# Performance work log

Hardware: AMD Instinct MI355X
Metric: run time of the kernel (lower is better)

The kernel has to match this reference:

```python
import jax, jax.numpy as jnp
import numpy as np

D_MODEL = 2048
D_STATE = 64
D_CONV = 4
EXPAND = 2
HEADDIM = 64
NGROUPS = 1
CHUNK = 64
D_INNER = D_MODEL * EXPAND          # 4096
NHEADS = D_INNER // HEADDIM         # 64
D_IN_PROJ = 2 * D_INNER + 2 * NGROUPS * D_STATE + NHEADS
BATCH, SEQLEN = 2, 4096
RMS_EPS = 1e-6


def elu_plus_one(x):
    return jax.nn.elu(x) + 1.0


def softplus(x):
    return jnp.where(x > 20, x, jnp.log1p(jnp.exp(x)))


def causal_conv1d(x, w, b):
    # x: (B, L, D), w: (K, D) depthwise kernel, b: (D,)
    Bsz, L, Dn = x.shape
    k = w.shape[0]
    xp = jnp.transpose(jnp.pad(x, ((0, 0), (k - 1, 0), (0, 0))), (0, 2, 1))  # (B, D, L+K-1)
    kern = jnp.transpose(w, (1, 0))[:, None, :]  # (D, 1, K)
    y = jax.lax.conv_general_dilated(xp, kern, (1,), 'VALID',
                                     feature_group_count=Dn,
                                     dimension_numbers=('NCH', 'OIH', 'NCH'))
    return jnp.transpose(y, (0, 2, 1)) + b


def ssd_chunked(q, k, v, a, chunk_size):
    # SSD / chunked linear attention with per-step scalar decay.
    # Recurrence: h_t = a_t * h_{t-1} + k_t v_t^T ; y_t = q_t @ h_t
    # q,k: (B,H,L,N); v: (B,H,L,P); a: (B,H,L) in (0,1)
    Bsz, H, L, N = q.shape
    S = chunk_size
    C = L // S
    qc = q.reshape(Bsz, H, C, S, N)
    kc = k.reshape(Bsz, H, C, S, N)
    vc = v.reshape(Bsz, H, C, S, -1)
    la = jnp.log(a).reshape(Bsz, H, C, S)
    cs = jnp.cumsum(la, axis=-1)                 # inclusive cumsum of log-decay within chunk
    causal = jnp.tril(jnp.ones((S, S), bool))
    # decay from position j to i (j<=i): exp(cs_i - cs_j)
    logdec = jnp.where(causal, cs[..., :, None] - cs[..., None, :], -jnp.inf)
    att = jnp.einsum('bhcsn,bhctn->bhcst', qc, kc) * jnp.exp(logdec)
    y_intra = jnp.einsum('bhcst,bhctp->bhcsp', att, vc)
    total = cs[..., -1]                           # (B,H,C) total log-decay per chunk
    k_scaled = kc * jnp.exp(total[..., None, None] - cs[..., None])
    states = jnp.einsum('bhcsn,bhcsp->bhcnp', k_scaled, vc)  # per-chunk state update
    d_t = jnp.moveaxis(jnp.exp(total), 2, 0)      # (C,B,H)
    s_t = jnp.moveaxis(states, 2, 0)              # (C,B,H,N,P)

    def step(h, inp):
        d, s = inp
        return d[..., None, None] * h + s, h      # emit state at chunk start

    _, h_prev = jax.lax.scan(step, jnp.zeros_like(s_t[0]), (d_t, s_t))
    h_prev = jnp.moveaxis(h_prev, 0, 2)           # (B,H,C,N,P)
    y_inter = jnp.einsum('bhcsn,bhcnp->bhcsp', qc * jnp.exp(cs)[..., None], h_prev)
    return (y_intra + y_inter).reshape(Bsz, H, L, -1)


def setup_inputs() -> dict:
    key = jax.random.key(0)
    k0, k1, k2, k3 = jax.random.split(key, 4)
    u = jax.random.normal(k0, (BATCH, SEQLEN, D_MODEL), jnp.float32)
    in_proj_w = jax.random.normal(k1, (D_MODEL, D_IN_PROJ), jnp.float32) / np.sqrt(D_MODEL)
    conv_weight = jax.random.normal(k2, (D_CONV, D_INNER), jnp.float32) / np.sqrt(D_CONV)
    conv_bias = jnp.zeros((D_INNER,), jnp.float32)
    A_log = jnp.log(jnp.linspace(1.0, 16.0, NHEADS)).astype(jnp.float32)
    dt_init = jnp.exp(jnp.linspace(np.log(0.001), np.log(0.1), NHEADS))
    dt_bias = (dt_init + jnp.log(-jnp.expm1(-dt_init))).astype(jnp.float32)
    D_param = jnp.ones((NHEADS,), jnp.float32)
    norm_scale = jnp.ones((D_INNER,), jnp.float32)
    out_proj_w = jax.random.normal(k3, (D_INNER, D_MODEL), jnp.float32) / np.sqrt(D_INNER)
    return dict(u=u, in_proj_w=in_proj_w, conv_weight=conv_weight, conv_bias=conv_bias,
                A_log=A_log, dt_bias=dt_bias, D_param=D_param, norm_scale=norm_scale,
                out_proj_w=out_proj_w)


def reference(u, in_proj_w, conv_weight, conv_bias, A_log, dt_bias, D_param, norm_scale, out_proj_w):
    Bsz, L, _ = u.shape
    zxBCdt = u @ in_proj_w
    splits = [D_INNER, 2 * D_INNER, 2 * D_INNER + NGROUPS * D_STATE, 2 * D_INNER + 2 * NGROUPS * D_STATE]
    z, x, B_proj, C_proj, dt_logits = jnp.split(zxBCdt, splits, axis=-1)
    x = jax.nn.silu(causal_conv1d(x, conv_weight, conv_bias))
    B_mat = elu_plus_one(B_proj.reshape(Bsz, L, NGROUPS, D_STATE))
    C_mat = elu_plus_one(C_proj.reshape(Bsz, L, NGROUPS, D_STATE))
    hpg = NHEADS // NGROUPS
    B_mat = jnp.repeat(B_mat, hpg, axis=2)   # (B,L,H,N)
    C_mat = jnp.repeat(C_mat, hpg, axis=2)
    dt = softplus(dt_logits + dt_bias)        # (B,L,H)
    a = jnp.exp(-dt * jnp.exp(A_log))         # (B,L,H), per-step decay
    x_heads = x.reshape(Bsz, L, NHEADS, HEADDIM)
    q = jnp.transpose(C_mat, (0, 2, 1, 3))
    k = jnp.transpose(B_mat, (0, 2, 1, 3))
    v = jnp.transpose(x_heads, (0, 2, 1, 3))
    a_t = jnp.transpose(a, (0, 2, 1))
    y = ssd_chunked(q, k, v, a_t, CHUNK)
    y = y + D_param[None, :, None, None] * v  # skip connection
    y = jnp.transpose(y, (0, 2, 1, 3)).reshape(Bsz, L, D_INNER)
    y = y * jax.lax.rsqrt(jnp.mean(y * y, axis=-1, keepdims=True) + RMS_EPS) * norm_scale
    y = y * jax.nn.silu(z)
    return y @ out_proj_w
```

## Files before the change

kernel.cpp:

```cpp
#include <hip/hip_runtime.h>
#include <hip/hip_bf16.h>
#include <cstdint>
#include <cstddef>

#define BATCH   2
#define SEQLEN  4096
#define DMODEL  2048
#define DINNER  4096
#define NHEADS  64
#define HEADDIM 64
#define DSTATE  64
#define CHUNK   64
#define NCHUNK  (SEQLEN/CHUNK)
#define DPROJ   8384
#define DPROJ_PAD 8448
#define MTOK    (BATCH*SEQLEN)
#define RMS_EPS 1e-6f

typedef __hip_bfloat16 bf16;
typedef __attribute__((ext_vector_type(8))) short bf16x8;
typedef __attribute__((ext_vector_type(4))) float f32x4;

__device__ __forceinline__ float siluf(float x) { return x / (1.f + expf(-x)); }
__device__ __forceinline__ float to_f(float x) { return x; }
__device__ __forceinline__ float to_f(bf16 x) { return __bfloat162float(x); }
__device__ __forceinline__ float bf2f(short s) { bf16 h; *(short*)&h = s; return __bfloat162float(h); }
__device__ __forceinline__ void from_f(float& d, float x) { d = x; }
__device__ __forceinline__ void from_f(bf16& d, float x) { d = __float2bfloat16(x); }

__device__ __forceinline__ void gload16(const void* g, void* l) {
  __builtin_amdgcn_global_load_lds(
      (const __attribute__((address_space(1))) void*)g,
      (__attribute__((address_space(3))) void*)l, 16, 0, 0);
}

template <int KT>
__global__ __launch_bounds__(1024, 4) void gemm_w16(
    const bf16* __restrict__ A, int lda,
    const bf16* __restrict__ BT, int ldb,
    bf16* __restrict__ C, int ldc, int gx) {
  __shared__ __align__(16) bf16 As[4 * 8192];
  __shared__ __align__(16) bf16 Bs[4 * 8192];
  const int tid  = threadIdx.x;
  const int lane = tid & 63;
  const int w    = tid >> 6;
  const int wm   = w >> 2;
  const int wn   = w & 3;
  const int lr   = lane & 15, lg = lane >> 4;
  const int fo   = 8 * (lg ^ ((lr >> 1) & 3));

  int nwg = gridDim.x;
  int bid = (int)blockIdx.x;
  int idx = (bid & 7) * (nwg >> 3) + (bid >> 3);
  int spos = idx % (8 * gx);
  const int m0 = ((idx / (8 * gx)) * 8 + (spos & 7)) * 256;
  const int n0 = (spos >> 3) * 256;

  const int srow = tid >> 2;
  const int ce   = 8 * ((tid & 3) ^ ((tid >> 3) & 3));
  const bf16* pA = A  + (size_t)(m0 + srow) * lda + ce;
  const bf16* pB = BT + (size_t)(n0 + srow) * ldb + ce;
  const int wofs = w * 512;
  const int aRd = (wm * 64 + lr) * 32 + fo;
  const int bRd = (wn * 64 + lr) * 32 + fo;

#define STAGE_A(kt) gload16(pA + ((kt) << 5), As + (((kt) & 3) << 13) + wofs)
#define STAGE_B(kt) gload16(pB + ((kt) << 5), Bs + (((kt) & 3) << 13) + wofs)

  f32x4 acc[4][4];
#pragma unroll
  for (int m = 0; m < 4; ++m)
#pragma unroll
    for (int n = 0; n < 4; ++n) acc[m][n] = (f32x4){0.f, 0.f, 0.f, 0.f};

#define KBODY(T, DOSTAGE, VMC) do {                                          \
    const bf16* Ab = As + (((T) & 3) << 13);                                 \
    const bf16* Bb = Bs + (((T) & 3) << 13);                                 \
    if (DOSTAGE) { STAGE_A((T) + 3); STAGE_B((T) + 3); }                     \
    bf16x8 bfv[4], af[4];                                                    \
    _Pragma("unroll")                                                        \
    for (int n = 0; n < 4; ++n) bfv[n] = *(const bf16x8*)&Bb[bRd + n * 512]; \
    _Pragma("unroll")                                                        \
    for (int m = 0; m < 4; ++m) af[m] = *(const bf16x8*)&Ab[aRd + m * 512];  \
    asm volatile("s_waitcnt lgkmcnt(0)" ::: "memory");                       \
    __builtin_amdgcn_sched_barrier(0);                                       \
    __builtin_amdgcn_s_setprio(1);                                           \
    _Pragma("unroll")                                                        \
    for (int m = 0; m < 4; ++m)                                              \
      _Pragma("unroll")                                                      \
      for (int n = 0; n < 4; ++n)                                            \
        acc[m][n] = __builtin_amdgcn_mfma_f32_16x16x32_bf16(af[m], bfv[n], acc[m][n], 0, 0, 0); \
    __builtin_amdgcn_s_setprio(0);                                           \
    asm volatile("s_waitcnt vmcnt(" #VMC ")" ::: "memory");                  \
    __builtin_amdgcn_s_barrier();                                            \
    __builtin_amdgcn_sched_barrier(0);                                       \
  } while (0)

  STAGE_A(0); STAGE_B(0); STAGE_A(1); STAGE_B(1); STAGE_A(2); STAGE_B(2);
  asm volatile("s_waitcnt vmcnt(4)" ::: "memory");
  __builtin_amdgcn_s_barrier();
  __builtin_amdgcn_sched_barrier(0);

#pragma unroll 4
  for (int t = 0; t < KT - 3; ++t) KBODY(t, true, 4);
  KBODY(KT - 3, false, 2);
  KBODY(KT - 2, false, 0);
  KBODY(KT - 1, false, 0);
#undef KBODY
#undef STAGE_A
#undef STAGE_B

  bf16* Ws = (w < 8 ? As : Bs) + (w & 7) * 4096;
#pragma unroll
  for (int m = 0; m < 4; ++m)
#pragma unroll
    for (int n = 0; n < 4; ++n)
#pragma unroll
      for (int reg = 0; reg < 4; ++reg) {
        int row = m * 16 + lg * 4 + reg;
        int slot = (n * 2 + (lr >> 3)) ^ (row & 7);
        Ws[row * 64 + slot * 8 + (lr & 7)] = __float2bfloat16(acc[m][n][reg]);
      }
  asm volatile("s_waitcnt lgkmcnt(0)" ::: "memory");
#pragma unroll
  for (int i = 0; i < 8; ++i) {
    int row = i * 8 + (lane >> 3);
    bf16x8 v = *(const bf16x8*)&Ws[row * 64 + ((lane & 7) ^ (lane >> 3)) * 8];
    int gcol = n0 + wn * 64 + (lane & 7) * 8;
    *(bf16x8*)&C[(size_t)(m0 + wm * 64 + row) * ldc + gcol] = v;
  }
}

template <typename TC, bool MASK, int KT>
__global__ __launch_bounds__(512, 2) void gemm_u(
    const bf16* __restrict__ A, int lda,
    const bf16* __restrict__ BT, int ldb,
    TC* __restrict__ C, int ldc, int Nvalid, int gx) {
  __shared__ __align__(16) bf16 As[4 * 8192];
  __shared__ __align__(16) bf16 Bs[4 * 8192];
  const int tid  = threadIdx.x;
  const int lane = tid & 63;
  const int w    = tid >> 6;
  const int wm   = w >> 2;
  const int wn   = w & 3;
  const int lr   = lane & 15, lg = lane >> 4;
  const int fo   = 8 * (lg ^ ((lr >> 1) & 3));

  int nwg = gridDim.x;
  int bid = (int)blockIdx.x;
  int idx = (bid & 7) * (nwg >> 3) + (bid >> 3);
  int spos = idx % (8 * gx);
  const int m0 = ((idx / (8 * gx)) * 8 + (spos & 7)) * 256;
  const int n0 = (spos >> 3) * 256;

  const int srow = tid >> 2;
  const int ce   = 8 * ((tid & 3) ^ ((tid >> 3) & 3));
  const bf16* pA0 = A  + (size_t)(m0 + srow)       * lda + ce;
  const bf16* pA1 = A  + (size_t)(m0 + 128 + srow) * lda + ce;
  const bf16* pB0 = BT + (size_t)(n0 + srow)       * ldb + ce;
  const bf16* pB1 = BT + (size_t)(n0 + 128 + srow) * ldb + ce;
  const int wofs = w * 512;
  const int aRd = (wm * 128 + lr) * 32 + fo;
  const int bRd = (wn * 64 + lr) * 32 + fo;

#define STAGE_A(kt) do {                                       \
    bf16* d_ = As + (((kt) & 3) << 13);  int kk_ = (kt) << 5;  \
    gload16(pA0 + kk_, d_ + wofs);                             \
    gload16(pA1 + kk_, d_ + 4096 + wofs);                      \
  } while (0)
#define STAGE_B(kt) do {                                       \
    bf16* d_ = Bs + (((kt) & 3) << 13);  int kk_ = (kt) << 5;  \
    gload16(pB0 + kk_, d_ + wofs);                             \
    gload16(pB1 + kk_, d_ + 4096 + wofs);                      \
  } while (0)

  f32x4 acc[8][4];
#pragma unroll
  for (int m = 0; m < 8; ++m)
#pragma unroll
    for (int n = 0; n < 4; ++n) acc[m][n] = (f32x4){0.f, 0.f, 0.f, 0.f};

#define KBODY(T, DOSTAGE, VMC) do {                                          \
    const bf16* Ab = As + (((T) & 3) << 13);                                 \
    const bf16* Bb = Bs + (((T) & 3) << 13);                                 \
    if (DOSTAGE) { STAGE_A((T) + 3); STAGE_B((T) + 3); }                     \
    bf16x8 bfv[4], af[4], ag[4];                                             \
    _Pragma("unroll")                                                        \
    for (int n = 0; n < 4; ++n) bfv[n] = *(const bf16x8*)&Bb[bRd + n * 512]; \
    _Pragma("unroll")                                                        \
    for (int m = 0; m < 4; ++m) af[m] = *(const bf16x8*)&Ab[aRd + m * 512];  \
    __builtin_amdgcn_sched_barrier(0);                                       \
    _Pragma("unroll")                                                        \
    for (int m = 0; m < 4; ++m) ag[m] = *(const bf16x8*)&Ab[aRd + (m + 4) * 512]; \
    asm volatile("s_waitcnt lgkmcnt(4)" ::: "memory");                       \
    __builtin_amdgcn_sched_barrier(0);                                       \
    __builtin_amdgcn_s_setprio(1);                                           \
    _Pragma("unroll")                                                        \
    for (int m = 0; m < 4; ++m)                                              \
      _Pragma("unroll")                                                      \
      for (int n = 0; n < 4; ++n)                                            \
        acc[m][n] = __builtin_amdgcn_mfma_f32_16x16x32_bf16(af[m], bfv[n], acc[m][n], 0, 0, 0); \
    asm volatile("s_waitcnt lgkmcnt(0)" ::: "memory");                       \
    __builtin_amdgcn_sched_barrier(0);                                       \
    _Pragma("unroll")                                                        \
    for (int m = 0; m < 4; ++m)                                              \
      _Pragma("unroll")                                                      \
      for (int n = 0; n < 4; ++n)                                            \
        acc[m + 4][n] = __builtin_amdgcn_mfma_f32_16x16x32_bf16(ag[m], bfv[n], acc[m + 4][n], 0, 0, 0); \
    __builtin_amdgcn_s_setprio(0);                                           \
    asm volatile("s_waitcnt vmcnt(" #VMC ")" ::: "memory");                  \
    __builtin_amdgcn_s_barrier();                                            \
    __builtin_amdgcn_sched_barrier(0);                                       \
  } while (0)

  STAGE_A(0); STAGE_B(0); STAGE_A(1); STAGE_B(1); STAGE_A(2); STAGE_B(2);
  asm volatile("s_waitcnt vmcnt(8)" ::: "memory");
  __builtin_amdgcn_s_barrier();
  __builtin_amdgcn_sched_barrier(0);

#pragma unroll 4
  for (int t = 0; t < KT - 3; ++t) KBODY(t, true, 8);
  KBODY(KT - 3, false, 4);
  KBODY(KT - 2, false, 0);
  KBODY(KT - 1, false, 0);
#undef KBODY
#undef STAGE_A
#undef STAGE_B

  if constexpr (__is_same(TC, bf16)) {
    bf16* Ws = (w < 4 ? As : Bs) + (w & 3) * 8192;
#pragma unroll
    for (int m = 0; m < 8; ++m)
#pragma unroll
      for (int n = 0; n < 4; ++n)
#pragma unroll
        for (int reg = 0; reg < 4; ++reg) {
          int row = m * 16 + lg * 4 + reg;
          int slot = (n * 2 + (lr >> 3)) ^ (row & 7);
          Ws[row * 64 + slot * 8 + (lr & 7)] = __float2bfloat16(acc[m][n][reg]);
        }
    asm volatile("s_waitcnt lgkmcnt(0)" ::: "memory");
#pragma unroll
    for (int i = 0; i < 16; ++i) {
      int row = i * 8 + (lane >> 3);
      bf16x8 v = *(const bf16x8*)&Ws[row * 64 + ((lane & 7) ^ (lane >> 3)) * 8];
      int gcol = n0 + wn * 64 + (lane & 7) * 8;
      if (!MASK || gcol < Nvalid)
        *(bf16x8*)&((bf16*)C)[(size_t)(m0 + wm * 128 + row) * ldc + gcol] = v;
    }
  } else {
#pragma unroll
    for (int m = 0; m < 8; ++m)
#pragma unroll
      for (int n = 0; n < 4; ++n) {
        int col = n0 + wn * 64 + n * 16 + lr;
        if (MASK && col >= Nvalid) continue;
        size_t rbase = (size_t)(m0 + wm * 128 + m * 16 + lg * 4);
#pragma unroll
        for (int reg = 0; reg < 4; ++reg)
          from_f(C[(rbase + reg) * ldc + col], acc[m][n][reg]);
      }
  }
}

template <typename TC, bool MASK>
__global__ __launch_bounds__(256) void gemm_mfma(
    const bf16* __restrict__ A, int lda,
    const bf16* __restrict__ BT, int ldb,
    TC* __restrict__ C, int ldc, int Kdim, int Nvalid) {
  __shared__ __align__(16) bf16 As[128 * 32];
  __shared__ __align__(16) bf16 Bs[128 * 32];
  const int tid  = threadIdx.x;
  const int lane = tid & 63;
  const int w    = tid >> 6;
  const int m0 = blockIdx.y * 128;
  const int n0 = blockIdx.x * 128;

  const int rs0 = w * 32 + (lane >> 2);
  const int ce  = 8 * ((lane & 3) ^ ((lane >> 2) & 3));
  const int fo  = 8 * ((lane >> 4) ^ (lane & 3));
  const int lr  = lane & 15, lg = lane >> 4;
  const int wr = w >> 1, wc = w & 1;

  f32x4 acc[4][4];
#pragma unroll
  for (int m = 0; m < 4; ++m)
#pragma unroll
    for (int n = 0; n < 4; ++n) acc[m][n] = (f32x4){0.f, 0.f, 0.f, 0.f};

  const size_t arow0 = (size_t)(m0 + rs0) * lda;
  const size_t arow1 = (size_t)(m0 + rs0 + 16) * lda;
  const size_t brow0 = (size_t)(n0 + rs0) * ldb;
  const size_t brow1 = (size_t)(n0 + rs0 + 16) * ldb;
  bf16* lA0 = &As[(w * 2 + 0) * 512];
  bf16* lA1 = &As[(w * 2 + 1) * 512];
  bf16* lB0 = &Bs[(w * 2 + 0) * 512];
  bf16* lB1 = &Bs[(w * 2 + 1) * 512];

  for (int k0 = 0; k0 < Kdim; k0 += 32) {
    __syncthreads();
    gload16(A + arow0 + k0 + ce, lA0);
    gload16(A + arow1 + k0 + ce, lA1);
    gload16(BT + brow0 + k0 + ce, lB0);
    gload16(BT + brow1 + k0 + ce, lB1);
    __syncthreads();
    bf16x8 af[4], bfr[4];
#pragma unroll
    for (int m = 0; m < 4; ++m)
      af[m] = *(const bf16x8*)&As[(wr * 64 + m * 16 + lr) * 32 + fo];
#pragma unroll
    for (int n = 0; n < 4; ++n)
      bfr[n] = *(const bf16x8*)&Bs[(wc * 64 + n * 16 + lr) * 32 + fo];
#pragma unroll
    for (int m = 0; m < 4; ++m)
#pragma unroll
      for (int n = 0; n < 4; ++n)
        acc[m][n] = __builtin_amdgcn_mfma_f32_16x16x32_bf16(af[m], bfr[n], acc[m][n], 0, 0, 0);
  }

#pragma unroll
  for (int m = 0; m < 4; ++m)
#pragma unroll
    for (int n = 0; n < 4; ++n) {
      int col = n0 + wc * 64 + n * 16 + lr;
      if (MASK && col >= Nvalid) continue;
      size_t rbase = (size_t)(m0 + wr * 64 + m * 16 + lg * 4);
#pragma unroll
      for (int reg = 0; reg < 4; ++reg)
        from_f(C[(rbase + reg) * ldc + col], acc[m][n][reg]);
    }
}

__global__ __launch_bounds__(256) void cast_bf16_kernel(
    const float* __restrict__ x, bf16* __restrict__ y) {
  size_t i = ((size_t)blockIdx.x * 256 + threadIdx.x) * 4;
  float4 v = *(const float4*)(x + i);
  y[i + 0] = __float2bfloat16(v.x);
  y[i + 1] = __float2bfloat16(v.y);
  y[i + 2] = __float2bfloat16(v.z);
  y[i + 3] = __float2bfloat16(v.w);
}

__global__ __launch_bounds__(256) void transpose_cast_kernel(
    const float* __restrict__ W, bf16* __restrict__ WT, int N, int K) {
  __shared__ float t[32][33];
  int n0 = blockIdx.x * 32, k0 = blockIdx.y * 32;
  int tx = threadIdx.x & 31, ty = threadIdx.x >> 5;
#pragma unroll
  for (int i = 0; i < 4; ++i) {
    int n = n0 + tx;
    t[ty + i * 8][tx] = (n < N) ? W[(size_t)(k0 + ty + i * 8) * N + n] : 0.f;
  }
  __syncthreads();
#pragma unroll
  for (int i = 0; i < 4; ++i) {
    int nn = ty + i * 8;
    WT[(size_t)(n0 + nn) * K + k0 + tx] = __float2bfloat16(t[tx][nn]);
  }
}

__global__ __launch_bounds__(256) void conv_silu_kernel(
    const bf16* __restrict__ zx, const float* __restrict__ cw,
    const float* __restrict__ cb, bf16* __restrict__ xc) {
  int idx = blockIdx.x * 256 + threadIdx.x;
  int d8 = (idx & 511) * 8;
  int m = idx >> 9;
  int l = m & (SEQLEN - 1);
  int b = m >> 12;
  float acc[8];
#pragma unroll
  for (int j = 0; j < 8; ++j) acc[j] = cb[d8 + j];
#pragma unroll
  for (int k = 0; k < 4; ++k) {
    int li = l - 3 + k;
    if (li >= 0) {
      bf16x8 xv = *(const bf16x8*)&zx[(size_t)(b * SEQLEN + li) * DPROJ + DINNER + d8];
      const float* cwp = cw + k * DINNER + d8;
#pragma unroll
      for (int j = 0; j < 8; ++j) acc[j] += bf2f(xv[j]) * cwp[j];
    }
  }
  bf16x8 o;
#pragma unroll
  for (int j = 0; j < 8; ++j) { bf16 h = __float2bfloat16(siluf(acc[j])); o[j] = *(short*)&h; }
  *(bf16x8*)&xc[(size_t)m * DINNER + d8] = o;
}

__global__ __launch_bounds__(256) void prep_cumsum_kernel(
    const bf16* __restrict__ zx, const float* __restrict__ A_log,
    const float* __restrict__ dt_bias, bf16* __restrict__ Bmb,
    bf16* __restrict__ Cmb, float* __restrict__ cs) {
  int bid = blockIdx.x;
  int c = bid & 63, b = bid >> 6;
  int m0 = b * SEQLEN + c * CHUNK;
  int tid = threadIdx.x;
  int s = tid >> 2, grp = (tid & 3) * 16;
  __shared__ float laT[64 * 65];
  __shared__ float segs[4][64];
  const bf16* row = zx + (size_t)(m0 + s) * DPROJ + 2 * DINNER;
  {
    union { bf16x8 v[2]; bf16 hh[16]; } u, o;
    u.v[0] = *(const bf16x8*)&row[grp];
    u.v[1] = *(const bf16x8*)&row[grp + 8];
#pragma unroll
    for (int i = 0; i < 16; ++i) {
      float bv = to_f(u.hh[i]);
      from_f(o.hh[i], bv > 0.f ? bv + 1.f : expf(bv));
    }
    *(bf16x8*)&Bmb[(size_t)(m0 + s) * 64 + grp] = o.v[0];
    *(bf16x8*)&Bmb[(size_t)(m0 + s) * 64 + grp + 8] = o.v[1];
    u.v[0] = *(const bf16x8*)&row[64 + grp];
    u.v[1] = *(const bf16x8*)&row[64 + grp + 8];
#pragma unroll
    for (int i = 0; i < 16; ++i) {
      float cv = to_f(u.hh[i]);
      from_f(o.hh[i], cv > 0.f ? cv + 1.f : expf(cv));
    }
    *(bf16x8*)&Cmb[(size_t)(m0 + s) * 64 + grp] = o.v[0];
    *(bf16x8*)&Cmb[(size_t)(m0 + s) * 64 + grp + 8] = o.v[1];
    u.v[0] = *(const bf16x8*)&row[128 + grp];
    u.v[1] = *(const bf16x8*)&row[128 + grp + 8];
#pragma unroll
    for (int i = 0; i < 16; ++i) {
      int j = grp + i;
      float dtl = to_f(u.hh[i]) + dt_bias[j];
      float dt = dtl > 20.f ? dtl : log1pf(expf(dtl));
      laT[j * 65 + s] = -dt * expf(A_log[j]);
    }
  }
  __syncthreads();
  int j = tid & 63, sg = tid >> 6;
  float p = 0.f;
#pragma unroll
  for (int i = 0; i < 16; ++i) p += laT[j * 65 + sg * 16 + i];
  segs[sg][j] = p;
  __syncthreads();
  float off = (sg > 0 ? segs[0][j] : 0.f) + (sg > 1 ? segs[1][j] : 0.f) +
              (sg > 2 ? segs[2][j] : 0.f);
  float acc = off;
#pragma unroll
  for (int i = 0; i < 16; ++i) {
    acc += laT[j * 65 + sg * 16 + i];
    cs[(size_t)(m0 + sg * 16 + i) * 64 + j] = acc;
  }
}

__global__ __launch_bounds__(256) void states_mfma(
    const bf16* __restrict__ Bmb, const bf16* __restrict__ xc,
    const float* __restrict__ cs, bf16* __restrict__ st) {
  int bid = blockIdx.x;
  int c = bid & 63, h = (bid >> 6) & 63, b = bid >> 12;
  int m0 = b * SEQLEN + c * CHUNK;
  int tid = threadIdx.x, lane = tid & 63, w = tid >> 6;
  int lr = lane & 15, lg = lane >> 4;
  __shared__ bf16 vT[64 * 72];
  __shared__ bf16 kT[64 * 72];
  int s4 = tid >> 2, c16 = (tid & 3) * 16;
  float cstot = cs[(size_t)(m0 + 63) * 64 + h];
  float ws = expf(cstot - cs[(size_t)(m0 + s4) * 64 + h]);
  {
    union { bf16x8 v[2]; bf16 hh[16]; } u;
    const bf16x8* pv = (const bf16x8*)&xc[(size_t)(m0 + s4) * DINNER + h * 64 + c16];
    u.v[0] = pv[0]; u.v[1] = pv[1];
#pragma unroll
    for (int i = 0; i < 16; ++i) vT[(c16 + i) * 72 + s4] = u.hh[i];
    const bf16x8* pk = (const bf16x8*)&Bmb[(size_t)(m0 + s4) * 64 + c16];
    u.v[0] = pk[0]; u.v[1] = pk[1];
#pragma unroll
    for (int i = 0; i < 16; ++i) kT[(c16 + i) * 72 + s4] = __float2bfloat16(to_f(u.hh[i]) * ws);
  }
  __syncthreads();
  f32x4 acc[4];
#pragma unroll
  for (int ct = 0; ct < 4; ++ct) acc[ct] = (f32x4){0.f, 0.f, 0.f, 0.f};
#pragma unroll
  for (int ks = 0; ks < 2; ++ks) {
    bf16x8 af = *(const bf16x8*)&vT[(w * 16 + lr) * 72 + ks * 32 + lg * 8];
#pragma unroll
    for (int ct = 0; ct < 4; ++ct) {
      bf16x8 bf_ = *(const bf16x8*)&kT[(ct * 16 + lr) * 72 + ks * 32 + lg * 8];
      acc[ct] = __builtin_amdgcn_mfma_f32_16x16x32_bf16(af, bf_, acc[ct], 0, 0, 0);
    }
  }
  size_t ob = (((size_t)(b * NHEADS + h)) * NCHUNK + c) * 4096;
#pragma unroll
  for (int ct = 0; ct < 4; ++ct) {
    int n = ct * 16 + lr;
#pragma unroll
    for (int r = 0; r < 4; ++r) {
      int p = w * 16 + lg * 4 + r;
      from_f(st[ob + (size_t)p * 64 + n], acc[ct][r]);
    }
  }
}

__global__ __launch_bounds__(256) void scan_kernel(
    const float* __restrict__ cs, bf16* __restrict__ st) {
  int bid = blockIdx.x;
  int bh = bid >> 2, qq = bid & 3;
  int b = bh >> 6, h = bh & 63;
  int tid = threadIdx.x;
  __shared__ float dec[64];
  if (tid < 64)
    dec[tid] = expf(cs[(size_t)(b * SEQLEN + tid * CHUNK + 63) * 64 + h]);
  int e0 = qq * 1024 + tid * 4;
  float hr[4] = {0.f, 0.f, 0.f, 0.f};
  size_t base = (size_t)bh * NCHUNK * 4096;
  typedef __attribute__((ext_vector_type(4))) short bf16x4;
  union U { bf16x4 v; bf16 hh[4]; };
  U buf[4];
  buf[0].v = *(bf16x4*)(st + base + 0 * 4096 + e0);
  buf[1].v = *(bf16x4*)(st + base + 1 * 4096 + e0);
  buf[2].v = *(bf16x4*)(st + base + 2 * 4096 + e0);
  __syncthreads();
#pragma unroll 4
  for (int c = 0; c < NCHUNK; ++c) {
    if (c + 3 < NCHUNK)
      buf[(c + 3) & 3].v = *(bf16x4*)(st + base + (size_t)(c + 3) * 4096 + e0);
    float d = dec[c];
    U out;
#pragma unroll
    for (int i = 0; i < 4; ++i) {
      float sv = to_f(buf[c & 3].hh[i]);
      from_f(out.hh[i], hr[i]);
      hr[i] = d * hr[i] + sv;
    }
    *(bf16x4*)(st + base + (size_t)c * 4096 + e0) = out.v;
  }
}

__global__ __launch_bounds__(256) void chunk_out_mfma(
    const bf16* __restrict__ Bmb, const bf16* __restrict__ Cmb,
    const bf16* __restrict__ xc, const float* __restrict__ cs,
    const bf16* __restrict__ st, const float* __restrict__ Dp,
    bf16* __restrict__ zx) {
  int bid = blockIdx.x;
  int c = bid & 63, h = (bid >> 6) & 63, b = bid >> 12;
  int m0 = b * SEQLEN + c * CHUNK;
  int tid = threadIdx.x, lane = tid & 63, w = tid >> 6;
  int lr = lane & 15, lg = lane >> 4;
  __shared__ bf16 qL[64 * 72];
  __shared__ bf16 kL[64 * 72];
  __shared__ bf16 A2[64 * 136];
  __shared__ bf16 B2[64 * 136];
  __shared__ float csl[64];
  int s4 = tid >> 2, c16 = (tid & 3) * 16;

  if (tid < 64) csl[tid] = cs[(size_t)(m0 + tid) * 64 + h];
  {
    const bf16x8* pq = (const bf16x8*)&Cmb[(size_t)(m0 + s4) * 64 + c16];
    *(bf16x8*)&qL[s4 * 72 + c16] = pq[0];
    *(bf16x8*)&qL[s4 * 72 + c16 + 8] = pq[1];
    const bf16x8* pk = (const bf16x8*)&Bmb[(size_t)(m0 + s4) * 64 + c16];
    *(bf16x8*)&kL[s4 * 72 + c16] = pk[0];
    *(bf16x8*)&kL[s4 * 72 + c16 + 8] = pk[1];
  }
  {
    union { bf16x8 v[2]; bf16 hh[16]; } u;
    const bf16x8* pv = (const bf16x8*)&xc[(size_t)(m0 + s4) * DINNER + h * 64 + c16];
    u.v[0] = pv[0]; u.v[1] = pv[1];
#pragma unroll
    for (int i = 0; i < 16; ++i) B2[(c16 + i) * 136 + s4] = u.hh[i];
  }
  {
    size_t hb = (((size_t)(b * NHEADS + h)) * NCHUNK + c) * 4096;
    const bf16x8* ph = (const bf16x8*)&st[hb + (size_t)s4 * 64 + c16];
    *(bf16x8*)&B2[s4 * 136 + 64 + c16] = ph[0];
    *(bf16x8*)&B2[s4 * 136 + 64 + c16 + 8] = ph[1];
  }
  __syncthreads();

  f32x4 acc1[4];
#pragma unroll
  for (int ct = 0; ct < 4; ++ct) acc1[ct] = (f32x4){0.f, 0.f, 0.f, 0.f};
#pragma unroll
  for (int ks = 0; ks < 2; ++ks) {
    bf16x8 af = *(const bf16x8*)&qL[(w * 16 + lr) * 72 + ks * 32 + lg * 8];
#pragma unroll
    for (int ct = 0; ct < 4; ++ct) {
      bf16x8 bf_ = *(const bf16x8*)&kL[(ct * 16 + lr) * 72 + ks * 32 + lg * 8];
      acc1[ct] = __builtin_amdgcn_mfma_f32_16x16x32_bf16(af, bf_, acc1[ct], 0, 0, 0);
    }
  }
  {
    float es = expf(csl[s4]);
    union { bf16x8 v[2]; bf16 hh[16]; } u;
    const bf16x8* pq = (const bf16x8*)&qL[s4 * 72 + c16];
    u.v[0] = pq[0]; u.v[1] = pq[1];
#pragma unroll
    for (int i = 0; i < 16; ++i) u.hh[i] = __float2bfloat16(to_f(u.hh[i]) * es);
    *(bf16x8*)&A2[s4 * 136 + 64 + c16] = u.v[0];
    *(bf16x8*)&A2[s4 * 136 + 64 + c16 + 8] = u.v[1];
  }
#pragma unroll
  for (int ct = 0; ct < 4; ++ct) {
    int t = ct * 16 + lr;
#pragma unroll
    for (int r = 0; r < 4; ++r) {
      int s = w * 16 + lg * 4 + r;
      float val = (t <= s) ? acc1[ct][r] * expf(csl[s] - csl[t]) : 0.f;
      A2[s * 136 + t] = __float2bfloat16(val);
    }
  }
  __syncthreads();

  float Dh = Dp[h];
  f32x4 acc2[4];
#pragma unroll
  for (int ct = 0; ct < 4; ++ct) {
    int p = ct * 16 + lr;
#pragma unroll
    for (int r = 0; r < 4; ++r)
      acc2[ct][r] = Dh * to_f(B2[p * 136 + (w * 16 + lg * 4 + r)]);
  }
#pragma unroll
  for (int ks = 0; ks < 4; ++ks) {
    bf16x8 af = *(const bf16x8*)&A2[(w * 16 + lr) * 136 + ks * 32 + lg * 8];
#pragma unroll
    for (int ct = 0; ct < 4; ++ct) {
      bf16x8 bf_ = *(const bf16x8*)&B2[(ct * 16 + lr) * 136 + ks * 32 + lg * 8];
      acc2[ct] = __builtin_amdgcn_mfma_f32_16x16x32_bf16(af, bf_, acc2[ct], 0, 0, 0);
    }
  }
  __syncthreads();
#pragma unroll
  for (int ct = 0; ct < 4; ++ct) {
    int p = ct * 16 + lr;
#pragma unroll
    for (int r = 0; r < 4; ++r)
      qL[(w * 16 + lg * 4 + r) * 72 + p] = __float2bfloat16(acc2[ct][r]);
  }
  __syncthreads();
  {
    const bf16x8* py = (const bf16x8*)&qL[s4 * 72 + c16];
    bf16x8* pg = (bf16x8*)&zx[(size_t)(m0 + s4) * DPROJ + DINNER + h * 64 + c16];
    pg[0] = py[0]; pg[1] = py[1];
  }
}

__global__ __launch_bounds__(256) void rmsnorm_gate_kernel(
    bf16* __restrict__ zx, const float* __restrict__ scale) {
  int m = blockIdx.x;
  int tid = threadIdx.x;
  bf16* row = zx + (size_t)m * DPROJ;
  float vals[16];
  float ss = 0.f;
#pragma unroll
  for (int g = 0; g < 2; ++g) {
    int d8 = (tid + g * 256) * 8;
    bf16x8 yv = *(const bf16x8*)&row[DINNER + d8];
#pragma unroll
    for (int j = 0; j < 8; ++j) {
      float y = bf2f(yv[j]);
      vals[g * 8 + j] = y;
      ss += y * y;
    }
  }
#pragma unroll
  for (int off = 32; off > 0; off >>= 1) ss += __shfl_down(ss, off, 64);
  __shared__ float red[4];
  if ((tid & 63) == 0) red[tid >> 6] = ss;
  __syncthreads();
  float tot = red[0] + red[1] + red[2] + red[3];
  float inv = rsqrtf(tot / (float)DINNER + RMS_EPS);
#pragma unroll
  for (int g = 0; g < 2; ++g) {
    int d8 = (tid + g * 256) * 8;
    bf16x8 zv = *(const bf16x8*)&row[d8];
    const float* sc = scale + d8;
    bf16x8 o;
#pragma unroll
    for (int j = 0; j < 8; ++j) {
      bf16 hh = __float2bfloat16(vals[g * 8 + j] * inv * sc[j] * siluf(bf2f(zv[j])));
      o[j] = *(short*)&hh;
    }
    *(bf16x8*)&row[DINNER + d8] = o;
  }
}

extern "C" void kernel_launch(void* const* d_in, const int* in_sizes, int n_in,
                              void* d_out, int out_size, void* d_ws, size_t ws_size,
                              hipStream_t stream) {
  const float* u       = (const float*)d_in[0];
  const float* Win     = (const float*)d_in[1];
  const float* cw      = (const float*)d_in[2];
  const float* cb      = (const float*)d_in[3];
  const float* A_log   = (const float*)d_in[4];
  const float* dt_bias = (const float*)d_in[5];
  const float* Dp      = (const float*)d_in[6];
  const float* nscale  = (const float*)d_in[7];
  const float* Wout    = (const float*)d_in[8];
  float* out = (float*)d_out;

  bf16* zx = (bf16*)d_ws;
  bf16* xc = zx + (size_t)MTOK * DPROJ;
  bf16* ub = xc;
  bf16* wT = xc + (size_t)MTOK * DINNER;
  bf16* Bmb = wT + (size_t)DPROJ_PAD * DMODEL;
  bf16* Cmb = Bmb + (size_t)MTOK * 64;
  float* cs = (float*)(Cmb + (size_t)MTOK * 64);
  bf16* st = (bf16*)d_out;

  cast_bf16_kernel<<<(MTOK * DMODEL) / (256 * 4), 256, 0, stream>>>(u, ub);
  transpose_cast_kernel<<<dim3(DPROJ_PAD / 32, DMODEL / 32), 256, 0, stream>>>(Win, wT, DPROJ, DMODEL);
  gemm_w16<DMODEL / 32><<<(2 * DINNER / 256) * (MTOK / 256), 1024, 0, stream>>>(
      ub, DMODEL, wT, DMODEL, zx, DPROJ, 2 * DINNER / 256);
  gemm_mfma<bf16, true><<<dim3(2, MTOK / 128), 256, 0, stream>>>(
      ub, DMODEL, wT + (size_t)(2 * DINNER) * DMODEL, DMODEL,
      zx + 2 * DINNER, DPROJ, DMODEL, 192);
  transpose_cast_kernel<<<dim3(DMODEL / 32, DINNER / 32), 256, 0, stream>>>(Wout, wT, DMODEL, DINNER);
  conv_silu_kernel<<<(MTOK * 512) / 256, 256, 0, stream>>>(zx, cw, cb, xc);
  prep_cumsum_kernel<<<BATCH * NCHUNK, 256, 0, stream>>>(zx, A_log, dt_bias, Bmb, Cmb, cs);
  states_mfma<<<BATCH * NHEADS * NCHUNK, 256, 0, stream>>>(Bmb, xc, cs, st);
  scan_kernel<<<BATCH * NHEADS * 4, 256, 0, stream>>>(cs, st);
  chunk_out_mfma<<<BATCH * NHEADS * NCHUNK, 256, 0, stream>>>(Bmb, Cmb, xc, cs, st, Dp, zx);
  rmsnorm_gate_kernel<<<MTOK, 256, 0, stream>>>(zx, nscale);
  gemm_u<float, false, DINNER / 32><<<(DMODEL / 256) * (MTOK / 256), 512, 0, stream>>>(
      zx + DINNER, DPROJ, wT, DINNER, out, DMODEL, DMODEL, DMODEL / 256);
}
```

Baseline: 663.9 us.

## Double-buffer GEMM fragments, reuse 1024-thread GEMM for out-proj, tile conv rows

```diff
diff --git a/kernel.cpp b/kernel.cpp
--- a/kernel.cpp
+++ b/kernel.cpp
@@ -34,11 +34,11 @@
       (__attribute__((address_space(3))) void*)l, 16, 0, 0);
 }
 
-template <int KT>
+template <typename TC, int KT>
 __global__ __launch_bounds__(1024, 4) void gemm_w16(
     const bf16* __restrict__ A, int lda,
     const bf16* __restrict__ BT, int ldb,
-    bf16* __restrict__ C, int ldc, int gx) {
+    TC* __restrict__ C, int ldc, int gx) {
   __shared__ __align__(16) bf16 As[4 * 8192];
   __shared__ __align__(16) bf16 Bs[4 * 8192];
   const int tid  = threadIdx.x;
@@ -73,164 +73,62 @@
 #pragma unroll
     for (int n = 0; n < 4; ++n) acc[m][n] = (f32x4){0.f, 0.f, 0.f, 0.f};
 
-#define KBODY(T, DOSTAGE, VMC) do {                                          \
-    const bf16* Ab = As + (((T) & 3) << 13);                                 \
-    const bf16* Bb = Bs + (((T) & 3) << 13);                                 \
-    if (DOSTAGE) { STAGE_A((T) + 3); STAGE_B((T) + 3); }                     \
-    bf16x8 bfv[4], af[4];                                                    \
-    _Pragma("unroll")                                                        \
-    for (int n = 0; n < 4; ++n) bfv[n] = *(const bf16x8*)&Bb[bRd + n * 512]; \
-    _Pragma("unroll")                                                        \
-    for (int m = 0; m < 4; ++m) af[m] = *(const bf16x8*)&Ab[aRd + m * 512];  \
-    asm volatile("s_waitcnt lgkmcnt(0)" ::: "memory");                       \
-    __builtin_amdgcn_sched_barrier(0);                                       \
-    __builtin_amdgcn_s_setprio(1);                                           \
-    _Pragma("unroll")                                                        \
-    for (int m = 0; m < 4; ++m)                                              \
-      _Pragma("unroll")                                                      \
-      for (int n = 0; n < 4; ++n)                                            \
-        acc[m][n] = __builtin_amdgcn_mfma_f32_16x16x32_bf16(af[m], bfv[n], acc[m][n], 0, 0, 0); \
-    __builtin_amdgcn_s_setprio(0);                                           \
-    asm volatile("s_waitcnt vmcnt(" #VMC ")" ::: "memory");                  \
-    __builtin_amdgcn_s_barrier();                                            \
-    __builtin_amdgcn_sched_barrier(0);                                       \
+  bf16x8 fr[2][8];
+
+#define RDFRAG(P, SL) do {                                                    \
+    const bf16* Ab_ = As + ((SL) << 13);                                      \
+    const bf16* Bb_ = Bs + ((SL) << 13);                                      \
+    _Pragma("unroll")                                                         \
+    for (int n = 0; n < 4; ++n) fr[P][4 + n] = *(const bf16x8*)&Bb_[bRd + n * 512]; \
+    _Pragma("unroll")                                                         \
+    for (int m = 0; m < 4; ++m) fr[P][m] = *(const bf16x8*)&Ab_[aRd + m * 512]; \
+  } while (0)
+
+#define KB(T, P, DOSTAGE, DOPF, VMC) do {                                     \
+    if (DOSTAGE) { STAGE_A((T) + 3); STAGE_B((T) + 3); }                      \
+    asm volatile("s_waitcnt lgkmcnt(0)" ::: "memory");                        \
+    __builtin_amdgcn_sched_barrier(0);                                        \
+    __builtin_amdgcn_s_setprio(1);                                            \
+    _Pragma("unroll")                                                         \
+    for (int m = 0; m < 4; ++m)                                               \
+      _Pragma("unroll")                                                       \
+      for (int n = 0; n < 4; ++n)                                             \
+        acc[m][n] = __builtin_amdgcn_mfma_f32_16x16x32_bf16(fr[P][m], fr[P][4 + n], acc[m][n], 0, 0, 0); \
+    __builtin_amdgcn_s_setprio(0);                                            \
+    if (DOPF) {                                                               \
+      asm volatile("s_waitcnt vmcnt(" #VMC ")" ::: "memory");                 \
+      __builtin_amdgcn_sched_barrier(0);                                      \
+      RDFRAG(1 - (P), ((T) + 1) & 3);                                         \
+    }                                                                         \
+    __builtin_amdgcn_s_barrier();                                             \
+    __builtin_amdgcn_sched_barrier(0);                                        \
   } while (0)
 
   STAGE_A(0); STAGE_B(0); STAGE_A(1); STAGE_B(1); STAGE_A(2); STAGE_B(2);
   asm volatile("s_waitcnt vmcnt(4)" ::: "memory");
   __builtin_amdgcn_s_barrier();
   __builtin_amdgcn_sched_barrier(0);
-
-#pragma unroll 4
-  for (int t = 0; t < KT - 3; ++t) KBODY(t, true, 4);
-  KBODY(KT - 3, false, 2);
-  KBODY(KT - 2, false, 0);
-  KBODY(KT - 1, false, 0);
-#undef KBODY
+  RDFRAG(0, 0);
+
+  for (int t4 = 0; t4 < KT - 4; t4 += 4) {
+    KB(t4 + 0, 0, true, true, 4);
+    KB(t4 + 1, 1, true, true, 4);
+    KB(t4 + 2, 0, true, true, 4);
+    KB(t4 + 3, 1, true, true, 4);
+  }
+  KB(KT - 4, 0, true,  true,  4);
+  KB(KT - 3, 1, false, true,  2);
+  KB(KT - 2, 0, false, true,  0);
+  KB(KT - 1, 1, false, false, 0);
+#undef KB
+#undef RDFRAG
 #undef STAGE_A
 #undef STAGE_B
 
-  bf16* Ws = (w < 8 ? As : Bs) + (w & 7) * 4096;
-#pragma unroll
-  for (int m = 0; m < 4; ++m)
-#pragma unroll
-    for (int n = 0; n < 4; ++n)
-#pragma unroll
-      for (int reg = 0; reg < 4; ++reg) {
-        int row = m * 16 + lg * 4 + reg;
-        int slot = (n * 2 + (lr >> 3)) ^ (row & 7);
-        Ws[row * 64 + slot * 8 + (lr & 7)] = __float2bfloat16(acc[m][n][reg]);
-      }
-  asm volatile("s_waitcnt lgkmcnt(0)" ::: "memory");
-#pragma unroll
-  for (int i = 0; i < 8; ++i) {
-    int row = i * 8 + (lane >> 3);
-    bf16x8 v = *(const bf16x8*)&Ws[row * 64 + ((lane & 7) ^ (lane >> 3)) * 8];
-    int gcol = n0 + wn * 64 + (lane & 7) * 8;
-    *(bf16x8*)&C[(size_t)(m0 + wm * 64 + row) * ldc + gcol] = v;
-  }
-}
-
-template <typename TC, bool MASK, int KT>
-__global__ __launch_bounds__(512, 2) void gemm_u(
-    const bf16* __restrict__ A, int lda,
-    const bf16* __restrict__ BT, int ldb,
-    TC* __restrict__ C, int ldc, int Nvalid, int gx) {
-  __shared__ __align__(16) bf16 As[4 * 8192];
-  __shared__ __align__(16) bf16 Bs[4 * 8192];
-  const int tid  = threadIdx.x;
-  const int lane = tid & 63;
-  const int w    = tid >> 6;
-  const int wm   = w >> 2;
-  const int wn   = w & 3;
-  const int lr   = lane & 15, lg = lane >> 4;
-  const int fo   = 8 * (lg ^ ((lr >> 1) & 3));
-
-  int nwg = gridDim.x;
-  int bid = (int)blockIdx.x;
-  int idx = (bid & 7) * (nwg >> 3) + (bid >> 3);
-  int spos = idx % (8 * gx);
-  const int m0 = ((idx / (8 * gx)) * 8 + (spos & 7)) * 256;
-  const int n0 = (spos >> 3) * 256;
-
-  const int srow = tid >> 2;
-  const int ce   = 8 * ((tid & 3) ^ ((tid >> 3) & 3));
-  const bf16* pA0 = A  + (size_t)(m0 + srow)       * lda + ce;
-  const bf16* pA1 = A  + (size_t)(m0 + 128 + srow) * lda + ce;
-  const bf16* pB0 = BT + (size_t)(n0 + srow)       * ldb + ce;
-  const bf16* pB1 = BT + (size_t)(n0 + 128 + srow) * ldb + ce;
-  const int wofs = w * 512;
-  const int aRd = (wm * 128 + lr) * 32 + fo;
-  const int bRd = (wn * 64 + lr) * 32 + fo;
-
-#define STAGE_A(kt) do {                                       \
-    bf16* d_ = As + (((kt) & 3) << 13);  int kk_ = (kt) << 5;  \
-    gload16(pA0 + kk_, d_ + wofs);                             \
-    gload16(pA1 + kk_, d_ + 4096 + wofs);                      \
-  } while (0)
-#define STAGE_B(kt) do {                                       \
-    bf16* d_ = Bs + (((kt) & 3) << 13);  int kk_ = (kt) << 5;  \
-    gload16(pB0 + kk_, d_ + wofs);                             \
-    gload16(pB1 + kk_, d_ + 4096 + wofs);                      \
-  } while (0)
-
-  f32x4 acc[8][4];
-#pragma unroll
-  for (int m = 0; m < 8; ++m)
-#pragma unroll
-    for (int n = 0; n < 4; ++n) acc[m][n] = (f32x4){0.f, 0.f, 0.f, 0.f};
-
-#define KBODY(T, DOSTAGE, VMC) do {                                          \
-    const bf16* Ab = As + (((T) & 3) << 13);                                 \
-    const bf16* Bb = Bs + (((T) & 3) << 13);                                 \
-    if (DOSTAGE) { STAGE_A((T) + 3); STAGE_B((T) + 3); }                     \
-    bf16x8 bfv[4], af[4], ag[4];                                             \
-    _Pragma("unroll")                                                        \
-    for (int n = 0; n < 4; ++n) bfv[n] = *(const bf16x8*)&Bb[bRd + n * 512]; \
-    _Pragma("unroll")                                                        \
-    for (int m = 0; m < 4; ++m) af[m] = *(const bf16x8*)&Ab[aRd + m * 512];  \
-    __builtin_amdgcn_sched_barrier(0);                                       \
-    _Pragma("unroll")                                                        \
-    for (int m = 0; m < 4; ++m) ag[m] = *(const bf16x8*)&Ab[aRd + (m + 4) * 512]; \
-    asm volatile("s_waitcnt lgkmcnt(4)" ::: "memory");                       \
-    __builtin_amdgcn_sched_barrier(0);                                       \
-    __builtin_amdgcn_s_setprio(1);                                           \
-    _Pragma("unroll")                                                        \
-    for (int m = 0; m < 4; ++m)                                              \
-      _Pragma("unroll")                                                      \
-      for (int n = 0; n < 4; ++n)                                            \
-        acc[m][n] = __builtin_amdgcn_mfma_f32_16x16x32_bf16(af[m], bfv[n], acc[m][n], 0, 0, 0); \
-    asm volatile("s_waitcnt lgkmcnt(0)" ::: "memory");                       \
-    __builtin_amdgcn_sched_barrier(0);                                       \
-    _Pragma("unroll")                                                        \
-    for (int m = 0; m < 4; ++m)                                              \
-      _Pragma("unroll")                                                      \
-      for (int n = 0; n < 4; ++n)                                            \
-        acc[m + 4][n] = __builtin_amdgcn_mfma_f32_16x16x32_bf16(ag[m], bfv[n], acc[m + 4][n], 0, 0, 0); \
-    __builtin_amdgcn_s_setprio(0);                                           \
-    asm volatile("s_waitcnt vmcnt(" #VMC ")" ::: "memory");                  \
-    __builtin_amdgcn_s_barrier();                                            \
-    __builtin_amdgcn_sched_barrier(0);                                       \
-  } while (0)
-
-  STAGE_A(0); STAGE_B(0); STAGE_A(1); STAGE_B(1); STAGE_A(2); STAGE_B(2);
-  asm volatile("s_waitcnt vmcnt(8)" ::: "memory");
-  __builtin_amdgcn_s_barrier();
-  __builtin_amdgcn_sched_barrier(0);
-
-#pragma unroll 4
-  for (int t = 0; t < KT - 3; ++t) KBODY(t, true, 8);
-  KBODY(KT - 3, false, 4);
-  KBODY(KT - 2, false, 0);
-  KBODY(KT - 1, false, 0);
-#undef KBODY
-#undef STAGE_A
-#undef STAGE_B
-
   if constexpr (__is_same(TC, bf16)) {
-    bf16* Ws = (w < 4 ? As : Bs) + (w & 3) * 8192;
-#pragma unroll
-    for (int m = 0; m < 8; ++m)
+    bf16* Ws = (w < 8 ? As : Bs) + (w & 7) * 4096;
+#pragma unroll
+    for (int m = 0; m < 4; ++m)
 #pragma unroll
       for (int n = 0; n < 4; ++n)
 #pragma unroll
@@ -241,21 +139,19 @@
         }
     asm volatile("s_waitcnt lgkmcnt(0)" ::: "memory");
 #pragma unroll
-    for (int i = 0; i < 16; ++i) {
+    for (int i = 0; i < 8; ++i) {
       int row = i * 8 + (lane >> 3);
       bf16x8 v = *(const bf16x8*)&Ws[row * 64 + ((lane & 7) ^ (lane >> 3)) * 8];
       int gcol = n0 + wn * 64 + (lane & 7) * 8;
-      if (!MASK || gcol < Nvalid)
-        *(bf16x8*)&((bf16*)C)[(size_t)(m0 + wm * 128 + row) * ldc + gcol] = v;
+      *(bf16x8*)&((bf16*)C)[(size_t)(m0 + wm * 64 + row) * ldc + gcol] = v;
     }
   } else {
 #pragma unroll
-    for (int m = 0; m < 8; ++m)
+    for (int m = 0; m < 4; ++m)
 #pragma unroll
       for (int n = 0; n < 4; ++n) {
         int col = n0 + wn * 64 + n * 16 + lr;
-        if (MASK && col >= Nvalid) continue;
-        size_t rbase = (size_t)(m0 + wm * 128 + m * 16 + lg * 4);
+        size_t rbase = (size_t)(m0 + wm * 64 + m * 16 + lg * 4);
 #pragma unroll
         for (int reg = 0; reg < 4; ++reg)
           from_f(C[(rbase + reg) * ldc + col], acc[m][n][reg]);
@@ -364,26 +260,49 @@
     const float* __restrict__ cb, bf16* __restrict__ xc) {
   int idx = blockIdx.x * 256 + threadIdx.x;
   int d8 = (idx & 511) * 8;
-  int m = idx >> 9;
-  int l = m & (SEQLEN - 1);
-  int b = m >> 12;
-  float acc[8];
-#pragma unroll
-  for (int j = 0; j < 8; ++j) acc[j] = cb[d8 + j];
+  int g = idx >> 9;
+  int m0 = g * 4;
+  int l0 = m0 & (SEQLEN - 1);
+  int b = m0 >> 12;
+  bf16x8 rows[7];
+  bf16x8 zvec;
+#pragma unroll
+  for (int j = 0; j < 8; ++j) zvec[j] = 0;
+#pragma unroll
+  for (int r = 0; r < 7; ++r) {
+    int li = l0 - 3 + r;
+    rows[r] = (li >= 0)
+        ? *(const bf16x8*)&zx[(size_t)(b * SEQLEN + li) * DPROJ + DINNER + d8]
+        : zvec;
+  }
+  float cwv[4][8], cbv[8];
 #pragma unroll
   for (int k = 0; k < 4; ++k) {
-    int li = l - 3 + k;
-    if (li >= 0) {
-      bf16x8 xv = *(const bf16x8*)&zx[(size_t)(b * SEQLEN + li) * DPROJ + DINNER + d8];
-      const float* cwp = cw + k * DINNER + d8;
-#pragma unroll
-      for (int j = 0; j < 8; ++j) acc[j] += bf2f(xv[j]) * cwp[j];
-    }
-  }
-  bf16x8 o;
-#pragma unroll
-  for (int j = 0; j < 8; ++j) { bf16 h = __float2bfloat16(siluf(acc[j])); o[j] = *(short*)&h; }
-  *(bf16x8*)&xc[(size_t)m * DINNER + d8] = o;
+    float4 a = *(const float4*)(cw + k * DINNER + d8);
+    float4 bb = *(const float4*)(cw + k * DINNER + d8 + 4);
+    cwv[k][0] = a.x; cwv[k][1] = a.y; cwv[k][2] = a.z; cwv[k][3] = a.w;
+    cwv[k][4] = bb.x; cwv[k][5] = bb.y; cwv[k][6] = bb.z; cwv[k][7] = bb.w;
+  }
+  {
+    float4 a = *(const float4*)(cb + d8);
+    float4 bb = *(const float4*)(cb + d8 + 4);
+    cbv[0] = a.x; cbv[1] = a.y; cbv[2] = a.z; cbv[3] = a.w;
+    cbv[4] = bb.x; cbv[5] = bb.y; cbv[6] = bb.z; cbv[7] = bb.w;
+  }
+#pragma unroll
+  for (int j = 0; j < 4; ++j) {
+    float acc[8];
+#pragma unroll
+    for (int e = 0; e < 8; ++e) acc[e] = cbv[e];
+#pragma unroll
+    for (int k = 0; k < 4; ++k)
+#pragma unroll
+      for (int e = 0; e < 8; ++e) acc[e] += bf2f(rows[j + k][e]) * cwv[k][e];
+    bf16x8 o;
+#pragma unroll
+    for (int e = 0; e < 8; ++e) { bf16 h = __float2bfloat16(siluf(acc[e])); o[e] = *(short*)&h; }
+    *(bf16x8*)&xc[(size_t)(m0 + j) * DINNER + d8] = o;
+  }
 }
 
 __global__ __launch_bounds__(256) void prep_cumsum_kernel(
@@ -703,18 +622,18 @@
 
   cast_bf16_kernel<<<(MTOK * DMODEL) / (256 * 4), 256, 0, stream>>>(u, ub);
   transpose_cast_kernel<<<dim3(DPROJ_PAD / 32, DMODEL / 32), 256, 0, stream>>>(Win, wT, DPROJ, DMODEL);
-  gemm_w16<DMODEL / 32><<<(2 * DINNER / 256) * (MTOK / 256), 1024, 0, stream>>>(
+  gemm_w16<bf16, DMODEL / 32><<<(2 * DINNER / 256) * (MTOK / 256), 1024, 0, stream>>>(
       ub, DMODEL, wT, DMODEL, zx, DPROJ, 2 * DINNER / 256);
   gemm_mfma<bf16, true><<<dim3(2, MTOK / 128), 256, 0, stream>>>(
       ub, DMODEL, wT + (size_t)(2 * DINNER) * DMODEL, DMODEL,
       zx + 2 * DINNER, DPROJ, DMODEL, 192);
   transpose_cast_kernel<<<dim3(DMODEL / 32, DINNER / 32), 256, 0, stream>>>(Wout, wT, DMODEL, DINNER);
-  conv_silu_kernel<<<(MTOK * 512) / 256, 256, 0, stream>>>(zx, cw, cb, xc);
+  conv_silu_kernel<<<(MTOK / 4) * 512 / 256, 256, 0, stream>>>(zx, cw, cb, xc);
   prep_cumsum_kernel<<<BATCH * NCHUNK, 256, 0, stream>>>(zx, A_log, dt_bias, Bmb, Cmb, cs);
   states_mfma<<<BATCH * NHEADS * NCHUNK, 256, 0, stream>>>(Bmb, xc, cs, st);
   scan_kernel<<<BATCH * NHEADS * 4, 256, 0, stream>>>(cs, st);
   chunk_out_mfma<<<BATCH * NHEADS * NCHUNK, 256, 0, stream>>>(Bmb, Cmb, xc, cs, st, Dp, zx);
   rmsnorm_gate_kernel<<<MTOK, 256, 0, stream>>>(zx, nscale);
-  gemm_u<float, false, DINNER / 32><<<(DMODEL / 256) * (MTOK / 256), 512, 0, stream>>>(
-      zx + DINNER, DPROJ, wT, DINNER, out, DMODEL, DMODEL, DMODEL / 256);
-}
+  gemm_w16<float, DINNER / 32><<<(DMODEL / 256) * (MTOK / 256), 1024, 0, stream>>>(
+      zx + DINNER, DPROJ, wT, DINNER, out, DMODEL, DMODEL / 256);
+}
```

New measurement: 650.1 us. 1.02x faster.
